# Kernel optimization log

Measured on AMD Instinct MI355X. Metric: run time of the kernel, lower is better.

The kernel has to match this reference:

```python
import jax, jax.numpy as jnp
import numpy as np
import math

D, H, B, T = 1024, 16, 2, 2048
DH = D // H


def setup_inputs() -> dict:
    key = jax.random.key(0)
    ks = jax.random.split(key, 9)
    s = 1.0 / math.sqrt(D)
    x = jax.random.normal(ks[0], (B, T, D), dtype=jnp.float32)
    # True = masked position (masked_fill semantics); causal mask broadcast over b, h
    mask = jnp.triu(jnp.ones((T, T), dtype=bool), k=1)[None, None, :, :]
    wq = jax.random.normal(ks[1], (D, D), dtype=jnp.float32) * s
    bq = jnp.zeros((D,), dtype=jnp.float32)
    wk = jax.random.normal(ks[2], (D, D), dtype=jnp.float32) * s
    bk = jnp.zeros((D,), dtype=jnp.float32)
    wv = jax.random.normal(ks[3], (D, D), dtype=jnp.float32) * s
    bv = jnp.zeros((D,), dtype=jnp.float32)
    wo = jax.random.normal(ks[4], (D, D), dtype=jnp.float32) * s
    bo = jnp.zeros((D,), dtype=jnp.float32)
    return {"x": x, "mask": mask, "wq": wq, "bq": bq, "wk": wk, "bk": bk,
            "wv": wv, "bv": bv, "wo": wo, "bo": bo}


def _rotate_half(u):
    h = u.shape[-1] // 2
    return jnp.concatenate([-u[..., h:], u[..., :h]], axis=-1)


def _sincos(t, dh, dtype):
    pos = jnp.arange(t, dtype=dtype)[:, None]                    # [t, 1]
    inv = 1.0 / (10000.0 ** (jnp.arange(0, dh, 2, dtype=dtype) / dh))  # [dh/2]
    ang = pos * inv                                              # [t, dh/2]
    sin = jnp.repeat(jnp.sin(ang), 2, axis=-1)                   # [t, dh]
    cos = jnp.repeat(jnp.cos(ang), 2, axis=-1)
    return sin, cos


def reference(x, mask, wq, bq, wk, bk, wv, bv, wo, bo):
    b, t, d = x.shape
    h, dh = H, DH
    def heads(u):  # [b,t,d] -> [b,h,t,dh]
        return u.reshape(b, t, h, dh).transpose(0, 2, 1, 3)
    q = heads(x @ wq + bq)
    k = heads(x @ wk + bk)
    v = heads(x @ wv + bv)
    sin, cos = _sincos(t, dh, x.dtype)                           # [t, dh]
    q = q * cos + _rotate_half(q) * sin
    k = k * cos + _rotate_half(k) * sin
    a = jnp.einsum('bhqd,bhkd->bhqk', q, k) / jnp.sqrt(jnp.asarray(dh, x.dtype))
    a = jnp.where(mask, jnp.asarray(-10000.0, x.dtype), a)
    a = jax.nn.softmax(a, axis=-1)                               # dropout p=0.0 -> identity
    out = jnp.einsum('bhqk,bhkd->bhqd', a, v)
    out = out.transpose(0, 2, 1, 3).reshape(b, t, d)
    return out @ wo + bo
```

## Files before the change

kernel.cpp:

```cpp
#include <hip/hip_runtime.h>
#include <hip/hip_bf16.h>

#define DD 1024
#define HH 16
#define BB 2
#define TT 2048
#define DHH 64
#define MM (BB * TT)
#define NQT (TT / 64)
#define BKG 32

typedef __attribute__((ext_vector_type(8))) short bfrag;
typedef __attribute__((ext_vector_type(4))) float ffrag;

__device__ __forceinline__ unsigned short f2bf(float f) {
    __hip_bfloat16 h = __float2bfloat16(f);
    return *reinterpret_cast<unsigned short*>(&h);
}

__device__ __forceinline__ void gl_lds16(const unsigned short* g, unsigned short* l) {
    __builtin_amdgcn_global_load_lds(
        (const __attribute__((address_space(1))) unsigned int*)g,
        (__attribute__((address_space(3))) unsigned int*)l, 16, 0, 0);
}

__global__ __launch_bounds__(256) void prepass_kernel(
    const float* __restrict__ x, unsigned short* __restrict__ xb,
    const float* __restrict__ wq, const float* __restrict__ wk,
    const float* __restrict__ wv, const float* __restrict__ wo,
    unsigned short* __restrict__ oq, unsigned short* __restrict__ ok,
    unsigned short* __restrict__ ov, unsigned short* __restrict__ oo,
    float4* __restrict__ rope_tab)
{
    __shared__ float T[64][65];
    const int z = blockIdx.z;
    const int t = threadIdx.x;
    if (z == 4) {
        const int bid = blockIdx.y * 16 + blockIdx.x;
#pragma unroll
        for (int g = 0; g < 16; ++g) {
            int i = bid * 4096 + g * 256 + t;
            float4 v = ((const float4*)x)[i];
            ushort4 o;
            o.x = f2bf(v.x); o.y = f2bf(v.y); o.z = f2bf(v.z); o.w = f2bf(v.w);
            ((ushort4*)xb)[i] = o;
        }
        int idx = bid * 256 + t;
        int tpos = idx >> 5, i = idx & 31;
        float inv = __expf(-(float)i * (9.210340371976184f / 32.0f));
        float ang = (float)tpos * inv;
        float sv, cv;
        sincosf(ang, &sv, &cv);
        const float S = 0.125f * 1.4426950408889634f;
        rope_tab[idx] = make_float4(cv, sv, S * cv, S * sv);
        return;
    }
    const float* W    = (z == 0) ? wq : (z == 1) ? wk : (z == 2) ? wv : wo;
    unsigned short* O = (z == 0) ? oq : (z == 1) ? ok : (z == 2) ? ov : oo;
    const int n0 = blockIdx.x * 64, k0 = blockIdx.y * 64;
#pragma unroll
    for (int g = 0; g < 16; ++g) {
        int idx = g * 256 + t;
        int r = idx >> 6, c = idx & 63;
        T[c][r] = W[(size_t)(k0 + r) * DD + n0 + c];
    }
    __syncthreads();
#pragma unroll
    for (int g = 0; g < 16; ++g) {
        int idx = g * 256 + t;
        int r = idx >> 6, c = idx & 63;
        O[(size_t)(n0 + r) * DD + k0 + c] = f2bf(T[r][c]);
    }
}

__device__ __forceinline__ void gemm128(
    const unsigned short* __restrict__ X, const unsigned short* __restrict__ Wt,
    int m0, int n0, unsigned short* As, unsigned short* Bs, ffrag acc[4][4])
{
    const int t  = threadIdx.x;
    const int l  = t & 63, w = t >> 6;
    const int lm = l & 15, lq = l >> 4;
    const int wr = w >> 1, wc = w & 1;
    const int srow = l >> 2;
    const int scol = (l & 3) * 8;
#pragma unroll
    for (int m = 0; m < 4; ++m)
#pragma unroll
        for (int n = 0; n < 4; ++n) acc[m][n] = (ffrag){0.f, 0.f, 0.f, 0.f};

    for (int k0 = 0; k0 < DD; k0 += BKG) {
#pragma unroll
        for (int it = 0; it < 2; ++it) {
            const int row = (w * 2 + it) * 16 + srow;
            gl_lds16(&X [(size_t)(m0 + row) * DD + k0 + scol], &As[(w * 2 + it) * 512]);
            gl_lds16(&Wt[(size_t)(n0 + row) * DD + k0 + scol], &Bs[(w * 2 + it) * 512]);
        }
        __syncthreads();
        bfrag a[4], b[4];
#pragma unroll
        for (int m = 0; m < 4; ++m)
            a[m] = *(const bfrag*)&As[(wr * 64 + m * 16 + lm) * BKG + lq * 8];
#pragma unroll
        for (int n = 0; n < 4; ++n)
            b[n] = *(const bfrag*)&Bs[(wc * 64 + n * 16 + lm) * BKG + lq * 8];
#pragma unroll
        for (int m = 0; m < 4; ++m)
#pragma unroll
            for (int n = 0; n < 4; ++n)
                acc[m][n] = __builtin_amdgcn_mfma_f32_16x16x32_bf16(a[m], b[n], acc[m][n], 0, 0, 0);
        __syncthreads();
    }
}

__global__ __launch_bounds__(256) void qkv_rope_kernel(
    const unsigned short* __restrict__ xb,
    const unsigned short* __restrict__ wt_qkv,
    const float* __restrict__ bq, const float* __restrict__ bk,
    const float* __restrict__ bv, const float4* __restrict__ rope_tab,
    unsigned short* __restrict__ Qh, unsigned short* __restrict__ Kh,
    unsigned short* __restrict__ Vh)
{
    __shared__ __align__(16) unsigned short As[128 * BKG];
    __shared__ __align__(16) unsigned short Bs[128 * BKG];
    const int n0 = blockIdx.x * 128, m0 = blockIdx.y * 128;
    ffrag acc[4][4];
    gemm128(xb, wt_qkv, m0, n0, As, Bs, acc);

    const int t  = threadIdx.x;
    const int l  = t & 63, w = t >> 6;
    const int lm = l & 15, lq = l >> 4;
    const int wr = w >> 1, wc = w & 1;
    const int ncol0 = n0 + wc * 64;
    const int which = ncol0 >> 10;
    const float* bias   = (which == 0) ? bq : (which == 1) ? bk : bv;
    unsigned short* Out = (which == 0) ? Qh : (which == 1) ? Kh : Vh;
    const int h = (ncol0 & 1023) >> 6;

    float bv4[4];
#pragma unroll
    for (int n = 0; n < 4; ++n) bv4[n] = bias[(ncol0 & 1023) + n * 16 + lm];

#pragma unroll
    for (int m = 0; m < 4; ++m) {
#pragma unroll
        for (int r = 0; r < 4; ++r) {
            const int row  = m0 + wr * 64 + m * 16 + lq * 4 + r;
            const int b    = row >> 11;
            const int tpos = row & 2047;
            const int bh   = b * HH + h;
#pragma unroll
            for (int n = 0; n < 4; ++n) {
                const int j = n * 16 + lm;
                float val = acc[m][n][r] + bv4[n];
                float outv;
                if (which < 2) {
                    float pair = acc[m][n ^ 2][r] + bv4[n ^ 2];
                    float rh   = (j < 32) ? -pair : pair;
                    float4 cs  = rope_tab[tpos * 32 + (j >> 1)];
                    outv = (which == 0) ? (val * cs.z + rh * cs.w)
                                        : (val * cs.x + rh * cs.y);
                } else {
                    outv = val;
                }
                Out[((size_t)bh * TT + tpos) * DHH + j] = f2bf(outv);
            }
        }
    }
}

__global__ __launch_bounds__(256) void attn_kernel(
    const unsigned short* __restrict__ Qh, const unsigned short* __restrict__ Kh,
    const unsigned short* __restrict__ Vh, unsigned short* __restrict__ attn_out)
{
    __shared__ __align__(16) unsigned short Ks[2][64][72];
    __shared__ __align__(16) unsigned short Vt[3][64][72];

    const int bh = blockIdx.y;
    const int t  = threadIdx.x;
    const int l  = t & 63, w = t >> 6;
    const int lm = l & 15, lq = l >> 4;
    const int g  = t >> 3;
    const int c0 = (t & 7) * 8;

    const unsigned short* Qb = Qh + (size_t)bh * TT * DHH;
    const unsigned short* Kb = Kh + (size_t)bh * TT * DHH;
    const unsigned short* Vb = Vh + (size_t)bh * TT * DHH;

    const bfrag onesf = (bfrag){0x3F80, 0x3F80, 0x3F80, 0x3F80,
                                0x3F80, 0x3F80, 0x3F80, 0x3F80};
    const int b = bh >> 4, h = bh & 15;
    const int srcA = (2 * (lq & 1)) * 16 + lm;
    const int srcB = srcA + 16;
    const bool sig = (lq >> 1) != 0;

#pragma unroll 1
    for (int pi = 0; pi < 2; ++pi) {
        const int qt  = (pi == 0) ? (NQT - 1 - (int)blockIdx.x) : (int)blockIdx.x;
        const int q0  = qt * 64, wm0 = q0 + w * 16;
        const int rowg = wm0 + lm;

        bfrag qf[2];
#pragma unroll
        for (int kc = 0; kc < 2; ++kc)
            qf[kc] = *(const bfrag*)&Qb[(size_t)(wm0 + lm) * DHH + kc * 32 + lq * 8];

        ffrag o[4];
#pragma unroll
        for (int s = 0; s < 4; ++s) o[s] = (ffrag){0.f, 0.f, 0.f, 0.f};
        ffrag lacc = (ffrag){0.f, 0.f, 0.f, 0.f};

        {
            uint4 ka  = *(const uint4*)&Kb[(size_t)(g) * DHH + c0];
            uint4 kb2 = *(const uint4*)&Kb[(size_t)(g + 32) * DHH + c0];
            uint4 va  = *(const uint4*)&Vb[(size_t)(2 * g) * DHH + c0];
            uint4 vb2 = *(const uint4*)&Vb[(size_t)(2 * g + 1) * DHH + c0];
            *(uint4*)&Ks[0][g][c0]      = ka;
            *(uint4*)&Ks[0][g + 32][c0] = kb2;
            const unsigned short* as = (const unsigned short*)&va;
            const unsigned short* bs = (const unsigned short*)&vb2;
#pragma unroll
            for (int j = 0; j < 8; ++j) {
                unsigned int wp = (unsigned int)as[j] | ((unsigned int)bs[j] << 16);
                const int dh = c0 + j;
                const int ch = (g >> 2) ^ ((dh >> 3) & 7);
                *(unsigned int*)&Vt[0][dh][ch * 8 + (g & 3) * 2] = wp;
            }
        }
        __syncthreads();

        const int nkt = qt + 1;
        bfrag paw_prev[2];
        int sl_prev = 2, sl_cur = 0, sl_next = 1;

#pragma unroll 1
        for (int kt = 0; kt < nkt; ++kt) {
            const int kcur = kt & 1;
            const bool pf = (kt < qt);
            uint4 ka, kb2, va, vb2;
            if (pf) {
                const int k1 = (kt + 1) * 64;
                ka  = *(const uint4*)&Kb[(size_t)(k1 + g) * DHH + c0];
                kb2 = *(const uint4*)&Kb[(size_t)(k1 + g + 32) * DHH + c0];
                va  = *(const uint4*)&Vb[(size_t)(k1 + 2 * g) * DHH + c0];
                vb2 = *(const uint4*)&Vb[(size_t)(k1 + 2 * g + 1) * DHH + c0];
            }
            const int k0 = kt * 64;

            float sv[4][4];
#pragma unroll
            for (int s = 0; s < 4; ++s) {
                ffrag sa = (ffrag){0.f, 0.f, 0.f, 0.f};
#pragma unroll
                for (int kc = 0; kc < 2; ++kc) {
                    bfrag kf = *(const bfrag*)&Ks[kcur][s * 16 + lm][kc * 32 + lq * 8];
                    sa = __builtin_amdgcn_mfma_f32_16x16x32_bf16(kf, qf[kc], sa, 0, 0, 0);
                }
#pragma unroll
                for (int r = 0; r < 4; ++r) sv[s][r] = sa[r];
            }

            if (kt > 0) {
#pragma unroll
                for (int kc = 0; kc < 2; ++kc) {
                    bfrag pa = paw_prev[kc];
#pragma unroll
                    for (int s = 0; s < 4; ++s) {
                        const int ch = (kc * 4 + lq) ^ ((s * 2 + (lm >> 3)) & 7);
                        bfrag vf = *(const bfrag*)&Vt[sl_prev][s * 16 + lm][ch * 8];
                        o[s] = __builtin_amdgcn_mfma_f32_16x16x32_bf16(pa, vf, o[s], 0, 0, 0);
                    }
                    lacc = __builtin_amdgcn_mfma_f32_16x16x32_bf16(pa, onesf, lacc, 0, 0, 0);
                }
            }

            if (kt == qt) {
#pragma unroll
                for (int s = 0; s < 4; ++s)
#pragma unroll
                    for (int r = 0; r < 4; ++r) {
                        const int col = k0 + s * 16 + lq * 4 + r;
                        if (col > rowg) sv[s][r] = -1e30f;
                    }
            }
#pragma unroll
            for (int s = 0; s < 4; ++s)
#pragma unroll
                for (int r = 0; r < 4; ++r)
                    sv[s][r] = __builtin_amdgcn_exp2f(sv[s][r]);

            unsigned int pk[8];
#pragma unroll
            for (int s = 0; s < 4; ++s)
#pragma unroll
                for (int p = 0; p < 2; ++p)
                    asm("v_cvt_pk_bf16_f32 %0, %1, %2"
                        : "=v"(pk[s * 2 + p])
                        : "v"(sv[s][2 * p]), "v"(sv[s][2 * p + 1]));

            uint4 paw[2];
#pragma unroll
            for (int kc = 0; kc < 2; ++kc)
#pragma unroll
                for (int m = 0; m < 4; ++m) {
                    const int src = (m & 2) ? srcB : srcA;
                    unsigned int w0 = (unsigned int)__shfl((int)pk[kc * 4 + (m & 1)], src, 64);
                    unsigned int w1 = (unsigned int)__shfl((int)pk[kc * 4 + 2 + (m & 1)], src, 64);
                    ((unsigned int*)&paw[kc])[m] = sig ? w1 : w0;
                }

            if (pf) {
                *(uint4*)&Ks[kcur ^ 1][g][c0]      = ka;
                *(uint4*)&Ks[kcur ^ 1][g + 32][c0] = kb2;
                const unsigned short* as = (const unsigned short*)&va;
                const unsigned short* bs = (const unsigned short*)&vb2;
#pragma unroll
                for (int j = 0; j < 8; ++j) {
                    unsigned int wp = (unsigned int)as[j] | ((unsigned int)bs[j] << 16);
                    const int dh = c0 + j;
                    const int ch = (g >> 2) ^ ((dh >> 3) & 7);
                    *(unsigned int*)&Vt[sl_next][dh][ch * 8 + (g & 3) * 2] = wp;
                }
            }
            __syncthreads();
            paw_prev[0] = *(const bfrag*)&paw[0];
            paw_prev[1] = *(const bfrag*)&paw[1];
            const int tmp = sl_prev; sl_prev = sl_cur; sl_cur = sl_next; sl_next = tmp;
        }

#pragma unroll
        for (int kc = 0; kc < 2; ++kc) {
            bfrag pa = paw_prev[kc];
#pragma unroll
            for (int s = 0; s < 4; ++s) {
                const int ch = (kc * 4 + lq) ^ ((s * 2 + (lm >> 3)) & 7);
                bfrag vf = *(const bfrag*)&Vt[sl_prev][s * 16 + lm][ch * 8];
                o[s] = __builtin_amdgcn_mfma_f32_16x16x32_bf16(pa, vf, o[s], 0, 0, 0);
            }
            lacc = __builtin_amdgcn_mfma_f32_16x16x32_bf16(pa, onesf, lacc, 0, 0, 0);
        }

#pragma unroll
        for (int r = 0; r < 4; ++r) {
            const int trow = wm0 + lq * 4 + r;
            const float linv = 1.0f / lacc[r];
#pragma unroll
            for (int s = 0; s < 4; ++s) {
                float ov = o[s][r] * linv;
                attn_out[(((size_t)b * TT + trow) * HH + h) * DHH + s * 16 + lm] = f2bf(ov);
            }
        }
        __syncthreads();
    }
}

__global__ __launch_bounds__(256) void oproj_kernel(
    const unsigned short* __restrict__ attn, const unsigned short* __restrict__ wto,
    const float* __restrict__ bo, float* __restrict__ out)
{
    __shared__ __align__(16) unsigned short As[128 * BKG];
    __shared__ __align__(16) unsigned short Bs[64 * BKG];
    const int n0 = blockIdx.x * 64, m0 = blockIdx.y * 128;
    const int t  = threadIdx.x;
    const int l  = t & 63, w = t >> 6;
    const int lm = l & 15, lq = l >> 4;

    ffrag acc[2][4];
#pragma unroll
    for (int m = 0; m < 2; ++m)
#pragma unroll
        for (int n = 0; n < 4; ++n) acc[m][n] = (ffrag){0.f, 0.f, 0.f, 0.f};

    for (int k0 = 0; k0 < DD; k0 += BKG) {
        {
            int c = t;
            gl_lds16(&attn[(size_t)(m0 + (c >> 2)) * DD + k0 + (c & 3) * 8], &As[c * 8]);
            c = t + 256;
            gl_lds16(&attn[(size_t)(m0 + (c >> 2)) * DD + k0 + (c & 3) * 8], &As[c * 8]);
            gl_lds16(&wto [(size_t)(n0 + (t >> 2)) * DD + k0 + (t & 3) * 8], &Bs[t * 8]);
        }
        __syncthreads();
        bfrag a[2], b[4];
#pragma unroll
        for (int m = 0; m < 2; ++m)
            a[m] = *(const bfrag*)&As[(w * 32 + m * 16 + lm) * BKG + lq * 8];
#pragma unroll
        for (int n = 0; n < 4; ++n)
            b[n] = *(const bfrag*)&Bs[(n * 16 + lm) * BKG + lq * 8];
#pragma unroll
        for (int m = 0; m < 2; ++m)
#pragma unroll
            for (int n = 0; n < 4; ++n)
                acc[m][n] = __builtin_amdgcn_mfma_f32_16x16x32_bf16(a[m], b[n], acc[m][n], 0, 0, 0);
        __syncthreads();
    }

#pragma unroll
    for (int n = 0; n < 4; ++n) {
        const int col = n0 + n * 16 + lm;
        const float bb = bo[col];
#pragma unroll
        for (int m = 0; m < 2; ++m)
#pragma unroll
            for (int r = 0; r < 4; ++r) {
                const int row = m0 + w * 32 + m * 16 + lq * 4 + r;
                out[(size_t)row * DD + col] = acc[m][n][r] + bb;
            }
    }
}

extern "C" void kernel_launch(void* const* d_in, const int* in_sizes, int n_in,
                              void* d_out, int out_size, void* d_ws, size_t ws_size,
                              hipStream_t stream) {
    const float* x  = (const float*)d_in[0];
    const float* wq = (const float*)d_in[2];
    const float* bq = (const float*)d_in[3];
    const float* wk = (const float*)d_in[4];
    const float* bk = (const float*)d_in[5];
    const float* wv = (const float*)d_in[6];
    const float* bv = (const float*)d_in[7];
    const float* wo = (const float*)d_in[8];
    const float* bo = (const float*)d_in[9];

    const size_t perT = (size_t)BB * HH * TT * DHH;
    const size_t perW = (size_t)DD * DD;
    unsigned short* xb   = (unsigned short*)d_ws;
    unsigned short* wtq  = xb  + perT;
    unsigned short* wtk  = wtq + perW;
    unsigned short* wtv  = wtk + perW;
    unsigned short* wto  = wtv + perW;
    unsigned short* Qh   = wto + perW;
    unsigned short* Kh   = Qh + perT;
    unsigned short* Vh   = Kh + perT;
    unsigned short* attn = Vh + perT;
    float4* rope_tab     = (float4*)(attn + perT);

    prepass_kernel<<<dim3(16, 16, 5), 256, 0, stream>>>(
        x, xb, wq, wk, wv, wo, wtq, wtk, wtv, wto, rope_tab);
    qkv_rope_kernel<<<dim3(24, 32), 256, 0, stream>>>(
        xb, wtq, bq, bk, bv, rope_tab, Qh, Kh, Vh);
    attn_kernel<<<dim3(NQT / 2, 32), 256, 0, stream>>>(Qh, Kh, Vh, attn);
    oproj_kernel<<<dim3(16, 32), 256, 0, stream>>>(attn, wto, bo, (float*)d_out);
}
```

Measured before the change: 221.6 us.

## Double GEMM K-tile with XOR-swizzled LDS; drop deferred PV pipelining in attention

The QKV and output-projection GEMMs now stage 64-wide K tiles instead of 32, using an XOR-swizzled LDS layout so fragment reads avoid bank conflicts. This halves the number of barrier-separated iterations, at the cost of twice the LDS per tile. The attention kernel stops deferring the P·V MFMAs by one iteration: it does them in the same iteration from the freshly written P, cutting the V buffers from three to two and removing the epilogue. That lowers LDS use and registers but gives up some overlap between the softmax and the PV MFMAs.

```diff
diff --git a/kernel.cpp b/kernel.cpp
--- a/kernel.cpp
+++ b/kernel.cpp
@@ -8,7 +8,7 @@
 #define DHH 64
 #define MM (BB * TT)
 #define NQT (TT / 64)
-#define BKG 32
+#define BKG 64
 
 typedef __attribute__((ext_vector_type(8))) short bfrag;
 typedef __attribute__((ext_vector_type(4))) float ffrag;
@@ -81,33 +81,38 @@
     const int l  = t & 63, w = t >> 6;
     const int lm = l & 15, lq = l >> 4;
     const int wr = w >> 1, wc = w & 1;
-    const int srow = l >> 2;
-    const int scol = (l & 3) * 8;
+    const int lrow = l >> 3;
+    const int scol = ((l & 7) ^ lrow) * 8;
 #pragma unroll
     for (int m = 0; m < 4; ++m)
 #pragma unroll
         for (int n = 0; n < 4; ++n) acc[m][n] = (ffrag){0.f, 0.f, 0.f, 0.f};
 
+    const int swz = lm & 7;
     for (int k0 = 0; k0 < DD; k0 += BKG) {
 #pragma unroll
-        for (int it = 0; it < 2; ++it) {
-            const int row = (w * 2 + it) * 16 + srow;
-            gl_lds16(&X [(size_t)(m0 + row) * DD + k0 + scol], &As[(w * 2 + it) * 512]);
-            gl_lds16(&Wt[(size_t)(n0 + row) * DD + k0 + scol], &Bs[(w * 2 + it) * 512]);
-        }
-        __syncthreads();
-        bfrag a[4], b[4];
-#pragma unroll
-        for (int m = 0; m < 4; ++m)
-            a[m] = *(const bfrag*)&As[(wr * 64 + m * 16 + lm) * BKG + lq * 8];
-#pragma unroll
-        for (int n = 0; n < 4; ++n)
-            b[n] = *(const bfrag*)&Bs[(wc * 64 + n * 16 + lm) * BKG + lq * 8];
-#pragma unroll
-        for (int m = 0; m < 4; ++m)
+        for (int it = 0; it < 4; ++it) {
+            const int rb = w * 32 + it * 8;
+            gl_lds16(&X [(size_t)(m0 + rb + lrow) * DD + k0 + scol], &As[rb * 64]);
+            gl_lds16(&Wt[(size_t)(n0 + rb + lrow) * DD + k0 + scol], &Bs[rb * 64]);
+        }
+        __syncthreads();
+#pragma unroll
+        for (int kc = 0; kc < 2; ++kc) {
+            const int ch = ((kc * 4 + lq) ^ swz) * 8;
+            bfrag a[4], b[4];
+#pragma unroll
+            for (int m = 0; m < 4; ++m)
+                a[m] = *(const bfrag*)&As[(wr * 64 + m * 16 + lm) * 64 + ch];
 #pragma unroll
             for (int n = 0; n < 4; ++n)
-                acc[m][n] = __builtin_amdgcn_mfma_f32_16x16x32_bf16(a[m], b[n], acc[m][n], 0, 0, 0);
+                b[n] = *(const bfrag*)&Bs[(wc * 64 + n * 16 + lm) * 64 + ch];
+#pragma unroll
+            for (int m = 0; m < 4; ++m)
+#pragma unroll
+                for (int n = 0; n < 4; ++n)
+                    acc[m][n] = __builtin_amdgcn_mfma_f32_16x16x32_bf16(a[m], b[n], acc[m][n], 0, 0, 0);
+        }
         __syncthreads();
     }
 }
@@ -173,7 +178,7 @@
     const unsigned short* __restrict__ Vh, unsigned short* __restrict__ attn_out)
 {
     __shared__ __align__(16) unsigned short Ks[2][64][72];
-    __shared__ __align__(16) unsigned short Vt[3][64][72];
+    __shared__ __align__(16) unsigned short Vt[2][64][72];
 
     const int bh = blockIdx.y;
     const int t  = threadIdx.x;
@@ -229,12 +234,9 @@
         __syncthreads();
 
         const int nkt = qt + 1;
-        bfrag paw_prev[2];
-        int sl_prev = 2, sl_cur = 0, sl_next = 1;
-
 #pragma unroll 1
         for (int kt = 0; kt < nkt; ++kt) {
-            const int kcur = kt & 1;
+            const int cur = kt & 1;
             const bool pf = (kt < qt);
             uint4 ka, kb2, va, vb2;
             if (pf) {
@@ -252,27 +254,12 @@
                 ffrag sa = (ffrag){0.f, 0.f, 0.f, 0.f};
 #pragma unroll
                 for (int kc = 0; kc < 2; ++kc) {
-                    bfrag kf = *(const bfrag*)&Ks[kcur][s * 16 + lm][kc * 32 + lq * 8];
+                    bfrag kf = *(const bfrag*)&Ks[cur][s * 16 + lm][kc * 32 + lq * 8];
                     sa = __builtin_amdgcn_mfma_f32_16x16x32_bf16(kf, qf[kc], sa, 0, 0, 0);
                 }
 #pragma unroll
                 for (int r = 0; r < 4; ++r) sv[s][r] = sa[r];
             }
-
-            if (kt > 0) {
-#pragma unroll
-                for (int kc = 0; kc < 2; ++kc) {
-                    bfrag pa = paw_prev[kc];
-#pragma unroll
-                    for (int s = 0; s < 4; ++s) {
-                        const int ch = (kc * 4 + lq) ^ ((s * 2 + (lm >> 3)) & 7);
-                        bfrag vf = *(const bfrag*)&Vt[sl_prev][s * 16 + lm][ch * 8];
-                        o[s] = __builtin_amdgcn_mfma_f32_16x16x32_bf16(pa, vf, o[s], 0, 0, 0);
-                    }
-                    lacc = __builtin_amdgcn_mfma_f32_16x16x32_bf16(pa, onesf, lacc, 0, 0, 0);
-                }
-            }
-
             if (kt == qt) {
 #pragma unroll
                 for (int s = 0; s < 4; ++s)
@@ -308,9 +295,22 @@
                     ((unsigned int*)&paw[kc])[m] = sig ? w1 : w0;
                 }
 
+#pragma unroll
+            for (int kc = 0; kc < 2; ++kc) {
+                bfrag pa = *(const bfrag*)&paw[kc];
+#pragma unroll
+                for (int s = 0; s < 4; ++s) {
+                    const int ch = (kc * 4 + lq) ^ ((s * 2 + (lm >> 3)) & 7);
+                    bfrag vf = *(const bfrag*)&Vt[cur][s * 16 + lm][ch * 8];
+                    o[s] = __builtin_amdgcn_mfma_f32_16x16x32_bf16(pa, vf, o[s], 0, 0, 0);
+                }
+                lacc = __builtin_amdgcn_mfma_f32_16x16x32_bf16(pa, onesf, lacc, 0, 0, 0);
+            }
+
             if (pf) {
-                *(uint4*)&Ks[kcur ^ 1][g][c0]      = ka;
-                *(uint4*)&Ks[kcur ^ 1][g + 32][c0] = kb2;
+                const int nxt = cur ^ 1;
+                *(uint4*)&Ks[nxt][g][c0]      = ka;
+                *(uint4*)&Ks[nxt][g + 32][c0] = kb2;
                 const unsigned short* as = (const unsigned short*)&va;
                 const unsigned short* bs = (const unsigned short*)&vb2;
 #pragma unroll
@@ -318,25 +318,10 @@
                     unsigned int wp = (unsigned int)as[j] | ((unsigned int)bs[j] << 16);
                     const int dh = c0 + j;
                     const int ch = (g >> 2) ^ ((dh >> 3) & 7);
-                    *(unsigned int*)&Vt[sl_next][dh][ch * 8 + (g & 3) * 2] = wp;
+                    *(unsigned int*)&Vt[nxt][dh][ch * 8 + (g & 3) * 2] = wp;
                 }
             }
             __syncthreads();
-            paw_prev[0] = *(const bfrag*)&paw[0];
-            paw_prev[1] = *(const bfrag*)&paw[1];
-            const int tmp = sl_prev; sl_prev = sl_cur; sl_cur = sl_next; sl_next = tmp;
-        }
-
-#pragma unroll
-        for (int kc = 0; kc < 2; ++kc) {
-            bfrag pa = paw_prev[kc];
-#pragma unroll
-            for (int s = 0; s < 4; ++s) {
-                const int ch = (kc * 4 + lq) ^ ((s * 2 + (lm >> 3)) & 7);
-                bfrag vf = *(const bfrag*)&Vt[sl_prev][s * 16 + lm][ch * 8];
-                o[s] = __builtin_amdgcn_mfma_f32_16x16x32_bf16(pa, vf, o[s], 0, 0, 0);
-            }
-            lacc = __builtin_amdgcn_mfma_f32_16x16x32_bf16(pa, onesf, lacc, 0, 0, 0);
         }
 
 #pragma unroll
@@ -363,6 +348,9 @@
     const int t  = threadIdx.x;
     const int l  = t & 63, w = t >> 6;
     const int lm = l & 15, lq = l >> 4;
+    const int lrow = l >> 3;
+    const int scol = ((l & 7) ^ lrow) * 8;
+    const int swz  = lm & 7;
 
     ffrag acc[2][4];
 #pragma unroll
@@ -371,26 +359,33 @@
         for (int n = 0; n < 4; ++n) acc[m][n] = (ffrag){0.f, 0.f, 0.f, 0.f};
 
     for (int k0 = 0; k0 < DD; k0 += BKG) {
-        {
-            int c = t;
-            gl_lds16(&attn[(size_t)(m0 + (c >> 2)) * DD + k0 + (c & 3) * 8], &As[c * 8]);
-            c = t + 256;
-            gl_lds16(&attn[(size_t)(m0 + (c >> 2)) * DD + k0 + (c & 3) * 8], &As[c * 8]);
-            gl_lds16(&wto [(size_t)(n0 + (t >> 2)) * DD + k0 + (t & 3) * 8], &Bs[t * 8]);
-        }
-        __syncthreads();
-        bfrag a[2], b[4];
-#pragma unroll
-        for (int m = 0; m < 2; ++m)
-            a[m] = *(const bfrag*)&As[(w * 32 + m * 16 + lm) * BKG + lq * 8];
-#pragma unroll
-        for (int n = 0; n < 4; ++n)
-            b[n] = *(const bfrag*)&Bs[(n * 16 + lm) * BKG + lq * 8];
-#pragma unroll
-        for (int m = 0; m < 2; ++m)
+#pragma unroll
+        for (int it = 0; it < 4; ++it) {
+            const int rb = w * 32 + it * 8;
+            gl_lds16(&attn[(size_t)(m0 + rb + lrow) * DD + k0 + scol], &As[rb * 64]);
+        }
+#pragma unroll
+        for (int it = 0; it < 2; ++it) {
+            const int rb = w * 16 + it * 8;
+            gl_lds16(&wto[(size_t)(n0 + rb + lrow) * DD + k0 + scol], &Bs[rb * 64]);
+        }
+        __syncthreads();
+#pragma unroll
+        for (int kc = 0; kc < 2; ++kc) {
+            const int ch = ((kc * 4 + lq) ^ swz) * 8;
+            bfrag a[2], b[4];
+#pragma unroll
+            for (int m = 0; m < 2; ++m)
+                a[m] = *(const bfrag*)&As[(w * 32 + m * 16 + lm) * 64 + ch];
 #pragma unroll
             for (int n = 0; n < 4; ++n)
-                acc[m][n] = __builtin_amdgcn_mfma_f32_16x16x32_bf16(a[m], b[n], acc[m][n], 0, 0, 0);
+                b[n] = *(const bfrag*)&Bs[(n * 16 + lm) * 64 + ch];
+#pragma unroll
+            for (int m = 0; m < 2; ++m)
+#pragma unroll
+                for (int n = 0; n < 4; ++n)
+                    acc[m][n] = __builtin_amdgcn_mfma_f32_16x16x32_bf16(a[m], b[n], acc[m][n], 0, 0, 0);
+        }
         __syncthreads();
     }
 
```

New measurement: 242.1 us. 1.09x slower.

## Drop software-pipelined PV stage and add MFMA priority hints in attention

Applied to the files above, without the earlier changes.

Removes the one-iteration lag where P·V for the previous key tile overlapped with QK^T of the current tile. PV now runs right after softmax in the same iteration, so the V tile buffer shrinks from three slots to two and the epilogue drain is gone. The MFMA sections are wrapped in s_setprio raises so the scheduler favours matrix work across waves. This trims LDS use and register pressure, which could raise occupancy, but it loses the intra-wave overlap between the exp/shuffle work and the PV MFMAs.

```diff
diff --git a/kernel.cpp b/kernel.cpp
--- a/kernel.cpp
+++ b/kernel.cpp
@@ -173,7 +173,7 @@
     const unsigned short* __restrict__ Vh, unsigned short* __restrict__ attn_out)
 {
     __shared__ __align__(16) unsigned short Ks[2][64][72];
-    __shared__ __align__(16) unsigned short Vt[3][64][72];
+    __shared__ __align__(16) unsigned short Vt[2][64][72];
 
     const int bh = blockIdx.y;
     const int t  = threadIdx.x;
@@ -229,12 +229,9 @@
         __syncthreads();
 
         const int nkt = qt + 1;
-        bfrag paw_prev[2];
-        int sl_prev = 2, sl_cur = 0, sl_next = 1;
-
 #pragma unroll 1
         for (int kt = 0; kt < nkt; ++kt) {
-            const int kcur = kt & 1;
+            const int cur = kt & 1;
             const bool pf = (kt < qt);
             uint4 ka, kb2, va, vb2;
             if (pf) {
@@ -247,32 +244,19 @@
             const int k0 = kt * 64;
 
             float sv[4][4];
+            __builtin_amdgcn_s_setprio(1);
 #pragma unroll
             for (int s = 0; s < 4; ++s) {
                 ffrag sa = (ffrag){0.f, 0.f, 0.f, 0.f};
 #pragma unroll
                 for (int kc = 0; kc < 2; ++kc) {
-                    bfrag kf = *(const bfrag*)&Ks[kcur][s * 16 + lm][kc * 32 + lq * 8];
+                    bfrag kf = *(const bfrag*)&Ks[cur][s * 16 + lm][kc * 32 + lq * 8];
                     sa = __builtin_amdgcn_mfma_f32_16x16x32_bf16(kf, qf[kc], sa, 0, 0, 0);
                 }
 #pragma unroll
                 for (int r = 0; r < 4; ++r) sv[s][r] = sa[r];
             }
-
-            if (kt > 0) {
-#pragma unroll
-                for (int kc = 0; kc < 2; ++kc) {
-                    bfrag pa = paw_prev[kc];
-#pragma unroll
-                    for (int s = 0; s < 4; ++s) {
-                        const int ch = (kc * 4 + lq) ^ ((s * 2 + (lm >> 3)) & 7);
-                        bfrag vf = *(const bfrag*)&Vt[sl_prev][s * 16 + lm][ch * 8];
-                        o[s] = __builtin_amdgcn_mfma_f32_16x16x32_bf16(pa, vf, o[s], 0, 0, 0);
-                    }
-                    lacc = __builtin_amdgcn_mfma_f32_16x16x32_bf16(pa, onesf, lacc, 0, 0, 0);
-                }
-            }
-
+            __builtin_amdgcn_s_setprio(0);
             if (kt == qt) {
 #pragma unroll
                 for (int s = 0; s < 4; ++s)
@@ -308,9 +292,24 @@
                     ((unsigned int*)&paw[kc])[m] = sig ? w1 : w0;
                 }
 
+            __builtin_amdgcn_s_setprio(1);
+#pragma unroll
+            for (int kc = 0; kc < 2; ++kc) {
+                bfrag pa = *(const bfrag*)&paw[kc];
+#pragma unroll
+                for (int s = 0; s < 4; ++s) {
+                    const int ch = (kc * 4 + lq) ^ ((s * 2 + (lm >> 3)) & 7);
+                    bfrag vf = *(const bfrag*)&Vt[cur][s * 16 + lm][ch * 8];
+                    o[s] = __builtin_amdgcn_mfma_f32_16x16x32_bf16(pa, vf, o[s], 0, 0, 0);
+                }
+                lacc = __builtin_amdgcn_mfma_f32_16x16x32_bf16(pa, onesf, lacc, 0, 0, 0);
+            }
+            __builtin_amdgcn_s_setprio(0);
+
             if (pf) {
-                *(uint4*)&Ks[kcur ^ 1][g][c0]      = ka;
-                *(uint4*)&Ks[kcur ^ 1][g + 32][c0] = kb2;
+                const int nxt = cur ^ 1;
+                *(uint4*)&Ks[nxt][g][c0]      = ka;
+                *(uint4*)&Ks[nxt][g + 32][c0] = kb2;
                 const unsigned short* as = (const unsigned short*)&va;
                 const unsigned short* bs = (const unsigned short*)&vb2;
 #pragma unroll
@@ -318,25 +317,10 @@
                     unsigned int wp = (unsigned int)as[j] | ((unsigned int)bs[j] << 16);
                     const int dh = c0 + j;
                     const int ch = (g >> 2) ^ ((dh >> 3) & 7);
-                    *(unsigned int*)&Vt[sl_next][dh][ch * 8 + (g & 3) * 2] = wp;
+                    *(unsigned int*)&Vt[nxt][dh][ch * 8 + (g & 3) * 2] = wp;
                 }
             }
             __syncthreads();
-            paw_prev[0] = *(const bfrag*)&paw[0];
-            paw_prev[1] = *(const bfrag*)&paw[1];
-            const int tmp = sl_prev; sl_prev = sl_cur; sl_cur = sl_next; sl_next = tmp;
-        }
-
-#pragma unroll
-        for (int kc = 0; kc < 2; ++kc) {
-            bfrag pa = paw_prev[kc];
-#pragma unroll
-            for (int s = 0; s < 4; ++s) {
-                const int ch = (kc * 4 + lq) ^ ((s * 2 + (lm >> 3)) & 7);
-                bfrag vf = *(const bfrag*)&Vt[sl_prev][s * 16 + lm][ch * 8];
-                o[s] = __builtin_amdgcn_mfma_f32_16x16x32_bf16(pa, vf, o[s], 0, 0, 0);
-            }
-            lacc = __builtin_amdgcn_mfma_f32_16x16x32_bf16(pa, onesf, lacc, 0, 0, 0);
         }
 
 #pragma unroll
```

Measured after the change: 220.2 us. No clear change (-0.6%).
